# Kernel tuning notes

Hardware: AMD Instinct MI355X
Metric: run time of the kernel (lower is better)

Reference implementation:

```python
import jax, jax.numpy as jnp
import numpy as np

NUM_ENT = 14541; NUM_REL = 237; NUM_EDGES = 544230
D = 200; B = 2048
IPERM = 1; IK_H = 20; IK_W = 10; NFILT = 96; KER = 9
FLAT = IK_H * 2 * IK_W * NFILT * IPERM
LEAKY = 0.2; EPS = 1e-5


def _chequer_perm(rng):
    # faithful reimplementation of RagatInteractE.get_chequer_perm
    ent_perm = np.stack([rng.permutation(D) for _ in range(IPERM)])
    rel_perm = np.stack([rng.permutation(D) for _ in range(IPERM)])
    comb = []
    for k in range(IPERM):
        temp = []; ei = 0; ri = 0
        for i in range(IK_H):
            for j in range(IK_W):
                ent_first = (k % 2 == 0) == (i % 2 == 0)
                if ent_first:
                    temp.append(ent_perm[k, ei]); ei += 1
                    temp.append(rel_perm[k, ri] + D); ri += 1
                else:
                    temp.append(rel_perm[k, ri] + D); ri += 1
                    temp.append(ent_perm[k, ei]); ei += 1
        comb.append(temp)
    return jnp.asarray(np.asarray(comb, dtype=np.int32))


def _bn1d(x, g, b):  # [N, C], training-mode batch stats (torch default)
    m = x.mean(0); v = x.var(0)
    return (x - m) / jnp.sqrt(v + EPS) * g + b


def _bn2d(x, g, b):  # [N, C, H, W]
    m = x.mean((0, 2, 3), keepdims=True); v = x.var((0, 2, 3), keepdims=True)
    return (x - m) / jnp.sqrt(v + EPS) * g[None, :, None, None] + b[None, :, None, None]


def _seg_softmax_agg(score, msg, seg, n):
    # segment softmax over edges grouped by destination node, then weighted scatter-add
    mx = jax.ops.segment_max(score, seg, num_segments=n)
    ex = jnp.exp(score - mx[seg])
    den = jax.ops.segment_sum(ex, seg, num_segments=n)
    alpha = ex / (den[seg] + 1e-16)
    return jax.ops.segment_sum(msg * alpha[:, None], seg, num_segments=n)


def setup_inputs() -> dict:
    key = jax.random.key(0)
    ks = jax.random.split(key, 20)
    f = lambda k, shp, s=0.1: jax.random.normal(k, shp, jnp.float32) * s
    rng = np.random.RandomState(0)
    return {
        'init_embed': f(ks[0], (NUM_ENT, D)),
        'init_rel': f(ks[1], (2 * NUM_REL, D)),
        'loop_rel': f(ks[2], (1, D)),
        'w_in': f(ks[3], (D, D)),
        'w_out': f(ks[4], (D, D)),
        'w_loop': f(ks[5], (D, D)),
        'w_rel': f(ks[6], (D, D)),
        'att_in': f(ks[7], (D,)),
        'att_out': f(ks[8], (D,)),
        'bn_conv_g': jnp.ones((D,), jnp.float32),
        'bn_conv_b': jnp.zeros((D,), jnp.float32),
        'conv_filt': f(ks[9], (NFILT, 1, KER, KER)),
        'bn0_g': jnp.ones((IPERM,), jnp.float32),
        'bn0_b': jnp.zeros((IPERM,), jnp.float32),
        'bn1_g': jnp.ones((NFILT * IPERM,), jnp.float32),
        'bn1_b': jnp.zeros((NFILT * IPERM,), jnp.float32),
        'fc_w': f(ks[10], (FLAT, D), 0.02),
        'fc_b': jnp.zeros((D,), jnp.float32),
        'bn2_g': jnp.ones((D,), jnp.float32),
        'bn2_b': jnp.zeros((D,), jnp.float32),
        'bias': jnp.zeros((NUM_ENT,), jnp.float32),
        'edge_index': jax.random.randint(ks[11], (2, NUM_EDGES), 0, NUM_ENT, jnp.int32),
        'edge_type': jnp.concatenate([
            jax.random.randint(ks[12], (NUM_EDGES // 2,), 0, NUM_REL, jnp.int32),
            jax.random.randint(ks[13], (NUM_EDGES // 2,), NUM_REL, 2 * NUM_REL, jnp.int32)]),
        'sub': jax.random.randint(ks[14], (B,), 0, NUM_ENT, jnp.int32),
        'rel': jax.random.randint(ks[15], (B,), 0, 2 * NUM_REL, jnp.int32),
        'chequer_perm': _chequer_perm(rng),
    }


def reference(init_embed, init_rel, loop_rel, w_in, w_out, w_loop, w_rel,
              att_in, att_out, bn_conv_g, bn_conv_b, conv_filt,
              bn0_g, bn0_b, bn1_g, bn1_b, fc_w, fc_b, bn2_g, bn2_b, bias,
              edge_index, edge_type, sub, rel, chequer_perm):
    # --- RagatConv (1 layer): relation-aware composition + edge attention + scatter-agg ---
    rel_full = jnp.concatenate([init_rel, loop_rel], 0)
    src, dst = edge_index[0], edge_index[1]
    comp = init_embed[dst] * rel_full[edge_type]          # [E, D] mult composition
    half = NUM_EDGES // 2
    msg_in = comp[:half] @ w_in                           # [E/2, D]
    msg_out = comp[half:] @ w_out
    s_in = jax.nn.leaky_relu((msg_in * att_in).sum(-1), LEAKY)
    s_out = jax.nn.leaky_relu((msg_out * att_out).sum(-1), LEAKY)
    agg_in = _seg_softmax_agg(s_in, msg_in, src[:half], NUM_ENT)
    agg_out = _seg_softmax_agg(s_out, msg_out, src[half:], NUM_ENT)
    loop_msg = (init_embed * loop_rel[0]) @ w_loop
    ent = (agg_in + agg_out + loop_msg) / 3.0
    ent = jnp.tanh(_bn1d(ent, bn_conv_g, bn_conv_b))      # [num_ent, D]
    rel_out = init_rel @ w_rel                            # [2*num_rel, D]

    # --- InteractE chequer-perm circular-conv scoring ---
    comb = jnp.concatenate([ent[sub], rel_out[rel]], 1)   # [B, 2D]
    cheq = comb[:, chequer_perm]                          # [B, IPERM, 2D]
    x = cheq.reshape(B, IPERM, 2 * IK_W, IK_H)
    x = _bn2d(x, bn0_g, bn0_b)
    p = KER // 2
    x = jnp.concatenate([x[..., -p:, :], x, x[..., :p, :]], axis=2)  # circular pad H
    x = jnp.concatenate([x[..., -p:], x, x[..., :p]], axis=3)        # circular pad W
    kern = jnp.tile(conv_filt, (IPERM, 1, 1, 1))          # [NFILT*IPERM, 1, K, K]
    x = jax.lax.conv_general_dilated(x, kern, (1, 1), 'VALID',
                                     dimension_numbers=('NCHW', 'OIHW', 'NCHW'),
                                     feature_group_count=IPERM)       # [B, 96, 20, 20]
    x = jax.nn.relu(_bn2d(x, bn1_g, bn1_b))
    x = x.reshape(B, FLAT)
    x = x @ fc_w + fc_b
    x = jax.nn.relu(_bn1d(x, bn2_g, bn2_b))               # [B, D]
    scores = x @ ent.T + bias                              # one_to_n scoring
    return jax.nn.sigmoid(scores)
```

## Files before the change

kernel.cpp:

```cpp
#include <hip/hip_runtime.h>
#include <hip/hip_bf16.h>

constexpr int DV     = 200;
constexpr int N_ENT  = 14541;
constexpr int N_EDGE = 544230;
constexpr int HALF_E = N_EDGE / 2;
constexpr int NSEG   = 2 * N_ENT;
constexpr int BB     = 2048;
constexpr int NF     = 96;
constexpr int FLATN  = 38400;
constexpr float LEAK = 0.2f;
constexpr float BEPS = 1e-5f;

typedef unsigned int u32;
typedef unsigned short u16;
typedef __attribute__((ext_vector_type(8))) short bf16x8;
typedef __attribute__((ext_vector_type(4))) float f32x4;
typedef __attribute__((ext_vector_type(4))) unsigned short u16x4;

constexpr size_t OFF_S    = 0;
constexpr size_t OFF_EID  = 544230;
constexpr size_t OFF_CNT  = 1088460;
constexpr size_t OFF_OFFS = 1117542;
constexpr size_t OFF_AGG  = 1146624;
constexpr size_t OFF_FC   = 6963218;
constexpr size_t ZERO_BEG = OFF_CNT;
constexpr size_t ZERO_END = OFF_FC + 409600;
constexpr size_t OFF_V    = 7372818;
constexpr size_t OFF_WTH  = 0;
constexpr size_t OFF_ENTH = 3840000;
constexpr size_t OFF_ENTL = 5352264;
constexpr size_t OFF_WTL  = 7373220;
constexpr size_t OFF_EPRE = 10281418;
constexpr size_t OFF_ENT  = 13189618;
constexpr size_t OFF_RELO = 16097818;
constexpr size_t OFF_CM   = 16192618;
constexpr size_t OFF_CV   = 16192818;
constexpr size_t OFF_CHEQ = 16193018;
constexpr size_t OFF_WT3H = 16193018;
constexpr size_t OFF_WT3L = 16261118;
constexpr size_t OFF_YH   = 16193020;
constexpr size_t OFF_YL   = 16406012;
constexpr size_t OFF_P0   = 17012218;
constexpr size_t OFF_ST0  = 17016314;
constexpr size_t OFF_CHP  = 17016316;
constexpr size_t OFF_B1SC = 17409532;
constexpr size_t OFF_B1BI = 17409628;
constexpr size_t OFF_XC   = 17819324;
constexpr size_t WS_WORDS = OFF_XC + 39321600;

__device__ inline float bf2f(u16 u) { return __uint_as_float(((u32)u) << 16); }
__device__ inline u16 f2bf(float f) {
    __hip_bfloat16 h = __float2bfloat16(f);
    return *reinterpret_cast<u16*>(&h);
}
__device__ inline void gl_lds16(const void* g, void* l) {
    __builtin_amdgcn_global_load_lds(
        (const __attribute__((address_space(1))) void*)g,
        (__attribute__((address_space(3))) void*)l, 16, 0, 0);
}

__global__ void k_vatt(const float* __restrict__ w_in, const float* __restrict__ w_out,
                       const float* __restrict__ att_in, const float* __restrict__ att_out,
                       float* __restrict__ v) {
    int t = blockIdx.x * 256 + threadIdx.x;
    if (t < DV) {
        float s = 0.f;
        for (int j = 0; j < DV; ++j) s += w_in[t * DV + j] * att_in[j];
        v[t] = s;
    } else if (t < 2 * DV) {
        int k = t - DV;
        float s = 0.f;
        for (int j = 0; j < DV; ++j) s += w_out[k * DV + j] * att_out[j];
        v[t] = s;
    }
}

__global__ void k_edge_score(const float* __restrict__ embed, const float* __restrict__ rel,
                             const int* __restrict__ eidx, const int* __restrict__ etype,
                             const float* __restrict__ v, float* __restrict__ s_all) {
    int gw = (blockIdx.x * 256 + threadIdx.x) >> 6;
    int lane = threadIdx.x & 63;
    if (gw >= N_EDGE) return;
    int e = gw;
    int dst = eidx[N_EDGE + e], et = etype[e];
    int dir = (e >= HALF_E);
    const float* vv = v + dir * DV;
    const float* er = embed + (size_t)dst * DV;
    const float* rr = rel + (size_t)et * DV;
    float acc = 0.f;
    for (int d = lane; d < DV; d += 64) acc += er[d] * rr[d] * vv[d];
    for (int off = 32; off > 0; off >>= 1) acc += __shfl_down(acc, off);
    if (lane == 0) {
        float s = acc > 0.f ? acc : LEAK * acc;
        s_all[e] = s;
    }
}

__global__ void k_hist(const int* __restrict__ eidx, u32* __restrict__ cnt) {
    int e = blockIdx.x * 256 + threadIdx.x;
    if (e >= N_EDGE) return;
    int seg = (e >= HALF_E ? N_ENT : 0) + eidx[e];
    atomicAdd(&cnt[seg], 1u);
}

__global__ void k_scan(u32* __restrict__ cnt, u32* __restrict__ offs) {
    __shared__ u32 s[256];
    __shared__ u32 base;
    if (threadIdx.x == 0) base = 0;
    __syncthreads();
    for (int c0 = 0; c0 < NSEG; c0 += 256) {
        int i = c0 + threadIdx.x;
        u32 vv = (i < NSEG) ? cnt[i] : 0;
        s[threadIdx.x] = vv;
        __syncthreads();
        for (int o = 1; o < 256; o <<= 1) {
            u32 t = (threadIdx.x >= (u32)o) ? s[threadIdx.x - o] : 0u;
            __syncthreads();
            s[threadIdx.x] += t;
            __syncthreads();
        }
        u32 exc = base + s[threadIdx.x] - vv;
        if (i < NSEG) { offs[i] = exc; cnt[i] = exc; }
        __syncthreads();
        if (threadIdx.x == 255) base += s[255];
        __syncthreads();
    }
}

__global__ void k_scatter(const int* __restrict__ eidx, u32* __restrict__ pos,
                          u32* __restrict__ eid) {
    int e = blockIdx.x * 256 + threadIdx.x;
    if (e >= N_EDGE) return;
    int seg = (e >= HALF_E ? N_ENT : 0) + eidx[e];
    u32 slot = atomicAdd(&pos[seg], 1u);
    eid[slot] = (u32)e;
}

__global__ void k_seg_agg(const float* __restrict__ embed, const float* __restrict__ rel,
                          const int* __restrict__ eidx, const int* __restrict__ etype,
                          const float* __restrict__ s_all, const u32* __restrict__ offs,
                          const u32* __restrict__ eid, float* __restrict__ aggC) {
    int gw = (blockIdx.x * 256 + threadIdx.x) >> 6;
    int lane = threadIdx.x & 63;
    if (gw >= NSEG) return;
    u32 beg = offs[gw];
    u32 end = (gw == NSEG - 1) ? (u32)N_EDGE : offs[gw + 1];
    int deg = (int)(end - beg);
    if (deg == 0) return;
    float m = -1e30f;
    for (int i = lane; i < deg; i += 64) m = fmaxf(m, s_all[eid[beg + i]]);
    for (int o = 32; o > 0; o >>= 1) m = fmaxf(m, __shfl_xor(m, o));
    float dsum = 0.f;
    for (int i = lane; i < deg; i += 64) dsum += expf(s_all[eid[beg + i]] - m);
    for (int o = 32; o > 0; o >>= 1) dsum += __shfl_xor(dsum, o);
    float inv = 1.f / (dsum + 1e-16f);
    float a0 = 0.f, a1 = 0.f, a2 = 0.f, a3 = 0.f;
    bool t3 = (lane < 8);
    for (int j = 0; j < deg; ++j) {
        int e = (int)eid[beg + j];
        float alpha = expf(s_all[e] - m) * inv;
        int dst = eidx[N_EDGE + e], et = etype[e];
        const float* er = embed + (size_t)dst * DV;
        const float* rr = rel + (size_t)et * DV;
        float p0 = er[lane] * rr[lane];
        float p1 = er[lane + 64] * rr[lane + 64];
        float p2 = er[lane + 128] * rr[lane + 128];
        float p3 = t3 ? er[lane + 192] * rr[lane + 192] : 0.f;
        a0 = fmaf(p0, alpha, a0);
        a1 = fmaf(p1, alpha, a1);
        a2 = fmaf(p2, alpha, a2);
        a3 = fmaf(p3, alpha, a3);
    }
    float* ag = aggC + (size_t)gw * DV;
    ag[lane] = a0;
    ag[lane + 64] = a1;
    ag[lane + 128] = a2;
    if (t3) ag[lane + 192] = a3;
}

__global__ void gemm_nn(const float* __restrict__ A, const float* __restrict__ B,
                        float* __restrict__ C, int M, int N, int K, int beta) {
    __shared__ float As[16][65];
    __shared__ float Bs[16][64];
    int bm = blockIdx.x * 64, bn = blockIdx.y * 64;
    int tx = threadIdx.x & 15, ty = threadIdx.x >> 4;
    float acc[4][4] = {};
    for (int k0 = 0; k0 < K; k0 += 16) {
        for (int i = threadIdx.x; i < 1024; i += 256) {
            int m = i >> 4, k = i & 15;
            int gm = bm + m, gk = k0 + k;
            As[k][m] = (gm < M && gk < K) ? A[(size_t)gm * K + gk] : 0.f;
        }
        for (int i = threadIdx.x; i < 1024; i += 256) {
            int k = i >> 6, n = i & 63;
            int gk = k0 + k, gn = bn + n;
            Bs[k][n] = (gk < K && gn < N) ? B[(size_t)gk * N + gn] : 0.f;
        }
        __syncthreads();
#pragma unroll
        for (int k = 0; k < 16; ++k) {
            float a[4], bv[4];
#pragma unroll
            for (int i = 0; i < 4; i++) a[i] = As[k][ty * 4 + i];
#pragma unroll
            for (int j = 0; j < 4; j++) bv[j] = Bs[k][tx * 4 + j];
#pragma unroll
            for (int i = 0; i < 4; i++)
#pragma unroll
                for (int j = 0; j < 4; j++) acc[i][j] += a[i] * bv[j];
        }
        __syncthreads();
    }
#pragma unroll
    for (int i = 0; i < 4; i++) {
        int r = bm + ty * 4 + i;
        if (r >= M) continue;
#pragma unroll
        for (int j = 0; j < 4; j++) {
            int c = bn + tx * 4 + j;
            if (c >= N) continue;
            size_t idx = (size_t)r * N + c;
            C[idx] = beta ? C[idx] + acc[i][j] : acc[i][j];
        }
    }
}

__global__ void k_wt3(const float* __restrict__ w_in, const float* __restrict__ w_out,
                      const float* __restrict__ w_loop,
                      u16* __restrict__ wTh, u16* __restrict__ wTl) {
    int i = blockIdx.x * 256 + threadIdx.x;
    if (i >= 3 * 200 * 224) return;
    int s = i / 44800, rem = i - s * 44800;
    int n = rem / 224, k = rem - n * 224;
    const float* w = (s == 0) ? w_in : (s == 1 ? w_out : w_loop);
    float v = (k < 200) ? w[k * 200 + n] : 0.f;
    u16 h = f2bf(v);
    wTh[i] = h;
    wTl[i] = f2bf(v - bf2f(h));
}

__global__ __launch_bounds__(256) void k_epre_mfma(const float* __restrict__ aggC,
        const float* __restrict__ embed, const float* __restrict__ lr,
        const u16* __restrict__ wTh, const u16* __restrict__ wTl,
        float* __restrict__ epre) {
    __shared__ __align__(16) char elds[26624];
    int tid = threadIdx.x;
    int w = tid >> 6, lane = tid & 63;
    int lrow = lane & 15, lkg = lane >> 4;
    int mw = blockIdx.x * 128 + w * 32;
    f32x4 acc[2][13] = {};
    for (int seg = 0; seg < 3; ++seg) {
        const float* Asrc = (seg == 0) ? aggC : (seg == 1 ? aggC + (size_t)N_ENT * DV : embed);
        const u16* bhg = wTh + seg * 44800;
        const u16* blg = wTl + seg * 44800;
        for (int kt = 0; kt < 7; ++kt) {
            int kb = kt * 32;
            __syncthreads();
            int kk = kb + lkg * 8;
            bool kval = (kt < 6) || (lkg < 1);
            bf16x8 ah[2], al[2];
#pragma unroll
            for (int mf = 0; mf < 2; ++mf) {
                int r = mw + mf * 16 + lrow; if (r > N_ENT - 1) r = N_ENT - 1;
                bf16x8 vh = {}, vl = {};
                if (kval) {
                    const float* ap = Asrc + (size_t)r * DV + kk;
#pragma unroll
                    for (int j = 0; j < 8; ++j) {
                        float v = ap[j];
                        if (seg == 2) v *= lr[kk + j];
                        u16 h = f2bf(v);
                        vh[j] = (short)h;
                        vl[j] = (short)f2bf(v - bf2f(h));
                    }
                }
                ah[mf] = vh; al[mf] = vl;
            }
#pragma unroll
            for (int q = 0; q < 4; ++q) {
                int bidx = q * 256 + w * 64;
                if (bidx < 832) {
                    int idx = bidx + lane;
                    int n = idx >> 2;
                    int slot = (idx & 3) ^ (n & 3);
                    size_t gsrc = (size_t)n * 224 + kb + slot * 8;
                    gl_lds16(bhg + gsrc, elds + bidx * 16);
                    gl_lds16(blg + gsrc, elds + 13312 + bidx * 16);
                }
            }
            __syncthreads();
#pragma unroll
            for (int nt = 0; nt < 13; ++nt) {
                int n = nt * 16 + lrow;
                int off = n * 64 + ((lkg ^ (n & 3)) << 4);
                bf16x8 bh = *reinterpret_cast<const bf16x8*>(elds + off);
                bf16x8 bl = *reinterpret_cast<const bf16x8*>(elds + 13312 + off);
#pragma unroll
                for (int mf = 0; mf < 2; ++mf) {
                    acc[mf][nt] = __builtin_amdgcn_mfma_f32_16x16x32_bf16(ah[mf], bh, acc[mf][nt], 0, 0, 0);
                    acc[mf][nt] = __builtin_amdgcn_mfma_f32_16x16x32_bf16(ah[mf], bl, acc[mf][nt], 0, 0, 0);
                    acc[mf][nt] = __builtin_amdgcn_mfma_f32_16x16x32_bf16(al[mf], bh, acc[mf][nt], 0, 0, 0);
                }
            }
        }
    }
#pragma unroll
    for (int mf = 0; mf < 2; ++mf)
#pragma unroll
        for (int nt = 0; nt < 13; ++nt) {
            int col = nt * 16 + lrow;
            if (col < DV) {
#pragma unroll
                for (int i = 0; i < 4; ++i) {
                    int r = mw + mf * 16 + lkg * 4 + i;
                    if (r < N_ENT) epre[(size_t)r * DV + col] = acc[mf][nt][i];
                }
            }
        }
}

__global__ void k_colstats(const float* __restrict__ X, int R,
                           float* __restrict__ cm, float* __restrict__ cv) {
    int col = blockIdx.x;
    __shared__ float rs[256], rss[256];
    float s = 0.f, ss = 0.f;
    for (int r = threadIdx.x; r < R; r += 256) {
        float x = X[(size_t)r * DV + col];
        s += x; ss += x * x;
    }
    rs[threadIdx.x] = s; rss[threadIdx.x] = ss;
    __syncthreads();
    for (int o = 128; o > 0; o >>= 1) {
        if (threadIdx.x < o) { rs[threadIdx.x] += rs[threadIdx.x + o]; rss[threadIdx.x] += rss[threadIdx.x + o]; }
        __syncthreads();
    }
    if (threadIdx.x == 0) {
        float m = rs[0] / R;
        cm[col] = m;
        cv[col] = rss[0] / R - m * m;
    }
}

__global__ void k_bn_ent(const float* __restrict__ epre, const float* __restrict__ cm,
                         const float* __restrict__ cv, const float* __restrict__ g,
                         const float* __restrict__ b, float* __restrict__ ent,
                         u16* __restrict__ eh, u16* __restrict__ el) {
    size_t i = (size_t)blockIdx.x * 256 + threadIdx.x;
    if (i >= (size_t)N_ENT * 208) return;
    int row = (int)(i / 208), col = (int)(i % 208);
    if (col < DV) {
        float val = (epre[(size_t)row * DV + col] - cm[col]) * rsqrtf(cv[col] + 9.f * BEPS) * g[col] + b[col];
        val = tanhf(val);
        ent[(size_t)row * DV + col] = val;
        u16 h = f2bf(val);
        eh[i] = h;
        el[i] = f2bf(val - bf2f(h));
    } else { eh[i] = 0; el[i] = 0; }
}

__global__ void k_bn2y(const float* __restrict__ fc, const float* __restrict__ cm,
                       const float* __restrict__ cv, const float* __restrict__ g,
                       const float* __restrict__ b, u16* __restrict__ yh,
                       u16* __restrict__ yl) {
    size_t i = (size_t)blockIdx.x * 256 + threadIdx.x;
    if (i >= (size_t)BB * 208) return;
    int row = (int)(i / 208), col = (int)(i % 208);
    if (col < DV) {
        float val = (fc[(size_t)row * DV + col] - cm[col]) * rsqrtf(cv[col] + BEPS) * g[col] + b[col];
        val = fmaxf(val, 0.f);
        u16 h = f2bf(val);
        yh[i] = h;
        yl[i] = f2bf(val - bf2f(h));
    } else { yh[i] = 0; yl[i] = 0; }
}

__global__ __launch_bounds__(256) void k_wt(const float* __restrict__ W,
                                            u16* __restrict__ Wth, u16* __restrict__ Wtl) {
    __shared__ float lds[64][65];
    int k0 = blockIdx.x * 64, n0 = blockIdx.y * 64;
    for (int idx = threadIdx.x; idx < 4096; idx += 256) {
        int kl = idx >> 6, nl = idx & 63;
        int gk = k0 + kl, gn = n0 + nl;
        lds[kl][nl] = (gn < DV) ? W[(size_t)gk * DV + gn] : 0.f;
    }
    __syncthreads();
    int nl = threadIdx.x >> 2, kq = threadIdx.x & 3;
    int gn = n0 + nl;
    if (gn >= DV) return;
    size_t base = (size_t)gn * FLATN + k0 + kq * 16;
    bf16x8 vh0, vh1, vl0, vl1;
#pragma unroll
    for (int j = 0; j < 8; ++j) {
        float w0 = lds[kq * 16 + j][nl];
        u16 h0 = f2bf(w0);
        vh0[j] = (short)h0; vl0[j] = (short)f2bf(w0 - bf2f(h0));
        float w1 = lds[kq * 16 + 8 + j][nl];
        u16 h1 = f2bf(w1);
        vh1[j] = (short)h1; vl1[j] = (short)f2bf(w1 - bf2f(h1));
    }
    *reinterpret_cast<bf16x8*>(Wth + base)     = vh0;
    *reinterpret_cast<bf16x8*>(Wth + base + 8) = vh1;
    *reinterpret_cast<bf16x8*>(Wtl + base)     = vl0;
    *reinterpret_cast<bf16x8*>(Wtl + base + 8) = vl1;
}

__global__ void k_cheq(const float* __restrict__ ent, const float* __restrict__ rel_out,
                       const int* __restrict__ sub, const int* __restrict__ rel,
                       const int* __restrict__ perm, float* __restrict__ cheq,
                       float* __restrict__ p0) {
    int b = blockIdx.x;
    int sb = sub[b], rb = rel[b];
    __shared__ float rs[256], rss[256];
    float s = 0.f, ss = 0.f;
    for (int i = threadIdx.x; i < 400; i += 256) {
        int p = perm[i];
        float v = (p < DV) ? ent[(size_t)sb * DV + p] : rel_out[(size_t)rb * DV + (p - DV)];
        cheq[(size_t)b * 400 + i] = v;
        s += v; ss += v * v;
    }
    rs[threadIdx.x] = s; rss[threadIdx.x] = ss;
    __syncthreads();
    for (int o = 128; o > 0; o >>= 1) {
        if (threadIdx.x < o) { rs[threadIdx.x] += rs[threadIdx.x + o]; rss[threadIdx.x] += rss[threadIdx.x + o]; }
        __syncthreads();
    }
    if (threadIdx.x == 0) { p0[b] = rs[0]; p0[BB + b] = rss[0]; }
}

__global__ void k_red_bn0(const float* __restrict__ p0, float* __restrict__ st) {
    __shared__ float rs[256], rss[256];
    float s = 0.f, ss = 0.f;
    for (int i = threadIdx.x; i < BB; i += 256) { s += p0[i]; ss += p0[BB + i]; }
    rs[threadIdx.x] = s; rss[threadIdx.x] = ss;
    __syncthreads();
    for (int o = 128; o > 0; o >>= 1) {
        if (threadIdx.x < o) { rs[threadIdx.x] += rs[threadIdx.x + o]; rss[threadIdx.x] += rss[threadIdx.x + o]; }
        __syncthreads();
    }
    if (threadIdx.x == 0) { st[0] = rs[0]; st[1] = rss[0]; }
}

__global__ __launch_bounds__(384, 4) void k_conv(const float* __restrict__ cheq,
                                              const float* __restrict__ st,
                                              const float* __restrict__ g0, const float* __restrict__ b0,
                                              const float* __restrict__ filt,
                                              __hip_bfloat16* __restrict__ xconv,
                                              float* __restrict__ chp) {
    int t = threadIdx.x;
    int img = t / 192;
    int tl = t - img * 192;
    int b = blockIdx.x * 2 + img;
    __shared__ float pad[2][784];
    __shared__ float flds[7968];
    __shared__ float red[384];
    for (int i = t; i < 7776; i += 384) {
        int f = i / 81, q = i - f * 81;
        flds[f * 83 + q] = filt[i];
    }
    const float N0 = (float)BB * 400.f;
    float m = st[0] / N0;
    float va = st[1] / N0 - m * m;
    float sg = rsqrtf(va + BEPS) * g0[0];
    float sb = b0[0] - m * sg;
    for (int i = t; i < 1568; i += 384) {
        int im = i / 784, j = i - im * 784;
        int h = j / 28, w2 = j % 28;
        int r = (h + 16) % 20, c = (w2 + 16) % 20;
        pad[im][j] = cheq[(size_t)(blockIdx.x * 2 + im) * 400 + r * 20 + c] * sg + sb;
    }
    __syncthreads();
    int f = tl % 96, hp = tl / 96;
    const float* fbase = flds + f * 83;
    const float* mypad = pad[img];
    float cs = 0.f, css = 0.f;
    u16* xo = (u16*)xconv + (size_t)b * FLATN + f * 400 + hp * 200;
    for (int rt = 0; rt < 10; ++rt) {
        int y = hp * 10 + rt;
        float acc[20];
#pragma unroll
        for (int x = 0; x < 20; ++x) acc[x] = 0.f;
        for (int dy = 0; dy < 9; ++dy) {
            float pr[28];
            const float4* prow = reinterpret_cast<const float4*>(&mypad[(y + dy) * 28]);
#pragma unroll
            for (int qv = 0; qv < 7; ++qv) {
                float4 v4 = prow[qv];
                pr[qv * 4 + 0] = v4.x; pr[qv * 4 + 1] = v4.y;
                pr[qv * 4 + 2] = v4.z; pr[qv * 4 + 3] = v4.w;
            }
            float fw[9];
#pragma unroll
            for (int dx = 0; dx < 9; ++dx) fw[dx] = fbase[dy * 9 + dx];
#pragma unroll
            for (int dx = 0; dx < 9; ++dx)
#pragma unroll
                for (int x = 0; x < 20; ++x)
                    acc[x] = fmaf(pr[x + dx], fw[dx], acc[x]);
        }
#pragma unroll
        for (int x = 0; x < 20; ++x) { cs += acc[x]; css += acc[x] * acc[x]; }
#pragma unroll
        for (int jj = 0; jj < 5; ++jj) {
            u16x4 o;
#pragma unroll
            for (int q2 = 0; q2 < 4; ++q2) o[q2] = f2bf(acc[jj * 4 + q2]);
            *reinterpret_cast<u16x4*>(xo + rt * 20 + jj * 4) = o;
        }
    }
    red[t] = cs; __syncthreads();
    if (tl < 96) chp[(size_t)b * 192 + tl] = red[img * 192 + tl] + red[img * 192 + tl + 96];
    __syncthreads();
    red[t] = css; __syncthreads();
    if (tl < 96) chp[(size_t)b * 192 + 96 + tl] = red[img * 192 + tl] + red[img * 192 + tl + 96];
}

__global__ void k_bn1_final(const float* __restrict__ chp, const float* __restrict__ g1,
                            const float* __restrict__ b1, float* __restrict__ sc,
                            float* __restrict__ bi) {
    int c = blockIdx.x;
    __shared__ float rs[256], rss[256];
    float s = 0.f, ss = 0.f;
    for (int b = threadIdx.x; b < BB; b += 256) {
        s += chp[(size_t)b * 192 + c];
        ss += chp[(size_t)b * 192 + 96 + c];
    }
    rs[threadIdx.x] = s; rss[threadIdx.x] = ss;
    __syncthreads();
    for (int o = 128; o > 0; o >>= 1) {
        if (threadIdx.x < o) { rs[threadIdx.x] += rs[threadIdx.x + o]; rss[threadIdx.x] += rss[threadIdx.x + o]; }
        __syncthreads();
    }
    if (threadIdx.x == 0) {
        float N = (float)BB * 400.f;
        float m = rs[0] / N;
        float v = rss[0] / N - m * m;
        float s_ = rsqrtf(v + BEPS) * g1[c];
        sc[c] = s_;
        bi[c] = b1[c] - m * s_;
    }
}

__global__ __launch_bounds__(256) void k_fc_mfma(const u16* __restrict__ X,
        const u16* __restrict__ Wth, const u16* __restrict__ Wtl,
        const float* __restrict__ sc, const float* __restrict__ bi,
        float* __restrict__ outp) {
    __shared__ __align__(16) char blds[53248];
    int tid = threadIdx.x;
    int w = tid >> 6, lane = tid & 63;
    int lrow = lane & 15, lkg = lane >> 4;
    int mw = blockIdx.x * 128 + w * 32;
    int kbase = blockIdx.y * 1280;
    f32x4 acc[2][13] = {};
    for (int it = 0; it < 20; ++it) {
        int k0 = kbase + it * 64;
        __syncthreads();
        bf16x8 araw[2][2];
#pragma unroll
        for (int mf = 0; mf < 2; ++mf)
#pragma unroll
            for (int kt = 0; kt < 2; ++kt) {
                int r = mw + mf * 16 + lrow;
                int kk = k0 + kt * 32 + lkg * 8;
                araw[mf][kt] = *reinterpret_cast<const bf16x8*>(X + (size_t)r * FLATN + kk);
            }
#pragma unroll
        for (int q = 0; q < 7; ++q) {
            int bidx = q * 256 + w * 64;
            if (bidx < 1600) {
                int idx = bidx + lane;
                int n = idx >> 3;
                int slot = (idx & 7) ^ (n & 7);
                size_t gsrc = (size_t)n * FLATN + k0 + slot * 8;
                gl_lds16(Wth + gsrc, blds + bidx * 16);
                gl_lds16(Wtl + gsrc, blds + 26624 + bidx * 16);
            }
        }
        bf16x8 ah[2][2], al[2][2];
#pragma unroll
        for (int mf = 0; mf < 2; ++mf)
#pragma unroll
            for (int kt = 0; kt < 2; ++kt) {
                int kk = k0 + kt * 32 + lkg * 8;
                int c = kk / 400;
                float s_ = sc[c], b_ = bi[c];
                bf16x8 fh2, fl2;
#pragma unroll
                for (int j = 0; j < 8; ++j) {
                    float v = bf2f((u16)araw[mf][kt][j]);
                    v = fmaxf(fmaf(v, s_, b_), 0.f);
                    u16 h = f2bf(v);
                    fh2[j] = (short)h;
                    fl2[j] = (short)f2bf(v - bf2f(h));
                }
                ah[mf][kt] = fh2;
                al[mf][kt] = fl2;
            }
        __syncthreads();
#pragma unroll
        for (int nt = 0; nt < 13; ++nt) {
            int n = nt * 16 + lrow;
            int row = n * 128, nx = n & 7;
            int off0 = row + ((lkg ^ nx) << 4);
            int off1 = row + (((4 + lkg) ^ nx) << 4);
            bf16x8 bh0 = *reinterpret_cast<const bf16x8*>(blds + off0);
            bf16x8 bh1 = *reinterpret_cast<const bf16x8*>(blds + off1);
            bf16x8 bl0 = *reinterpret_cast<const bf16x8*>(blds + 26624 + off0);
            bf16x8 bl1 = *reinterpret_cast<const bf16x8*>(blds + 26624 + off1);
#pragma unroll
            for (int mf = 0; mf < 2; ++mf) {
                acc[mf][nt] = __builtin_amdgcn_mfma_f32_16x16x32_bf16(ah[mf][0], bh0, acc[mf][nt], 0, 0, 0);
                acc[mf][nt] = __builtin_amdgcn_mfma_f32_16x16x32_bf16(ah[mf][1], bh1, acc[mf][nt], 0, 0, 0);
                acc[mf][nt] = __builtin_amdgcn_mfma_f32_16x16x32_bf16(ah[mf][0], bl0, acc[mf][nt], 0, 0, 0);
                acc[mf][nt] = __builtin_amdgcn_mfma_f32_16x16x32_bf16(ah[mf][1], bl1, acc[mf][nt], 0, 0, 0);
                acc[mf][nt] = __builtin_amdgcn_mfma_f32_16x16x32_bf16(al[mf][0], bh0, acc[mf][nt], 0, 0, 0);
                acc[mf][nt] = __builtin_amdgcn_mfma_f32_16x16x32_bf16(al[mf][1], bh1, acc[mf][nt], 0, 0, 0);
            }
        }
    }
#pragma unroll
    for (int mf = 0; mf < 2; ++mf)
#pragma unroll
        for (int nt = 0; nt < 13; ++nt) {
            int col = nt * 16 + lrow;
            if (col < DV) {
#pragma unroll
                for (int i = 0; i < 4; ++i) {
                    int r = mw + mf * 16 + lkg * 4 + i;
                    unsafeAtomicAdd(&outp[(size_t)r * DV + col], acc[mf][nt][i]);
                }
            }
        }
}

__global__ __launch_bounds__(256) void k_sc_mfma(const u16* __restrict__ Yh, const u16* __restrict__ Yl,
        const u16* __restrict__ Eh, const u16* __restrict__ El,
        const float* __restrict__ bias, float* __restrict__ outp) {
    __shared__ __align__(16) char elds[32768];
    int tid = threadIdx.x;
    int w = tid >> 6, lane = tid & 63;
    int lrow = lane & 15, lkg = lane >> 4;
    int mw = blockIdx.x * 128 + w * 32;
    int bn = blockIdx.y * 256;
    f32x4 acc[2][16] = {};
    bf16x8 zv = {};
    for (int kt = 0; kt < 7; ++kt) {
        int kbase = kt * 32;
        __syncthreads();
        int kk = kbase + lkg * 8;
        bool kval = (kt < 6) || (lkg < 2);
        bf16x8 ah[2], al[2];
#pragma unroll
        for (int mf = 0; mf < 2; ++mf) {
            int r = mw + mf * 16 + lrow;
            size_t off = (size_t)r * 208 + kk;
            ah[mf] = kval ? *reinterpret_cast<const bf16x8*>(Yh + off) : zv;
            al[mf] = kval ? *reinterpret_cast<const bf16x8*>(Yl + off) : zv;
        }
#pragma unroll
        for (int q = 0; q < 4; ++q) {
            int bidx = q * 256 + w * 64;
            int idx = bidx + lane;
            int n = idx >> 2;
            int slot = (idx & 3) ^ (n & 3);
            int gn = bn + n; if (gn > N_ENT - 1) gn = N_ENT - 1;
            size_t gsrc = (size_t)gn * 208 + kbase + slot * 8;
            gl_lds16(Eh + gsrc, elds + bidx * 16);
            gl_lds16(El + gsrc, elds + 16384 + bidx * 16);
        }
        __syncthreads();
#pragma unroll
        for (int nt = 0; nt < 16; ++nt) {
            int n = nt * 16 + lrow;
            int off = n * 64 + ((lkg ^ (n & 3)) << 4);
            bf16x8 bh = *reinterpret_cast<const bf16x8*>(elds + off);
            bf16x8 bl = *reinterpret_cast<const bf16x8*>(elds + 16384 + off);
            acc[0][nt] = __builtin_amdgcn_mfma_f32_16x16x32_bf16(ah[0], bh, acc[0][nt], 0, 0, 0);
            acc[0][nt] = __builtin_amdgcn_mfma_f32_16x16x32_bf16(ah[0], bl, acc[0][nt], 0, 0, 0);
            acc[0][nt] = __builtin_amdgcn_mfma_f32_16x16x32_bf16(al[0], bh, acc[0][nt], 0, 0, 0);
            acc[1][nt] = __builtin_amdgcn_mfma_f32_16x16x32_bf16(ah[1], bh, acc[1][nt], 0, 0, 0);
            acc[1][nt] = __builtin_amdgcn_mfma_f32_16x16x32_bf16(ah[1], bl, acc[1][nt], 0, 0, 0);
            acc[1][nt] = __builtin_amdgcn_mfma_f32_16x16x32_bf16(al[1], bh, acc[1][nt], 0, 0, 0);
        }
    }
#pragma unroll
    for (int mf = 0; mf < 2; ++mf)
#pragma unroll
        for (int nt = 0; nt < 16; ++nt) {
            int col = bn + nt * 16 + lrow;
            if (col < N_ENT) {
                float bv = bias[col];
#pragma unroll
                for (int i = 0; i < 4; ++i) {
                    int r = mw + mf * 16 + lkg * 4 + i;
                    float s = acc[mf][nt][i] + bv;
                    outp[(size_t)r * N_ENT + col] = 1.f / (1.f + expf(-s));
                }
            }
        }
}

extern "C" void kernel_launch(void* const* d_in, const int* in_sizes, int n_in,
                              void* d_out, int out_size, void* d_ws, size_t ws_size,
                              hipStream_t stream) {
    const float* init_embed = (const float*)d_in[0];
    const float* init_rel   = (const float*)d_in[1];
    const float* loop_rel   = (const float*)d_in[2];
    const float* w_in   = (const float*)d_in[3];
    const float* w_out  = (const float*)d_in[4];
    const float* w_loop = (const float*)d_in[5];
    const float* w_rel  = (const float*)d_in[6];
    const float* att_in  = (const float*)d_in[7];
    const float* att_out = (const float*)d_in[8];
    const float* bnc_g = (const float*)d_in[9];
    const float* bnc_b = (const float*)d_in[10];
    const float* filt  = (const float*)d_in[11];
    const float* g0 = (const float*)d_in[12];
    const float* b0 = (const float*)d_in[13];
    const float* g1 = (const float*)d_in[14];
    const float* b1 = (const float*)d_in[15];
    const float* fc_w = (const float*)d_in[16];
    const float* g2 = (const float*)d_in[18];
    const float* b2 = (const float*)d_in[19];
    const float* bias = (const float*)d_in[20];
    const int* eidx  = (const int*)d_in[21];
    const int* etype = (const int*)d_in[22];
    const int* sub   = (const int*)d_in[23];
    const int* rel   = (const int*)d_in[24];
    const int* perm  = (const int*)d_in[25];

    float* ws = (float*)d_ws;
    float* outp = (float*)d_out;
    if (ws_size < WS_WORDS * sizeof(float)) return;

    float* s_all  = ws + OFF_S;
    u32*   eid    = (u32*)(ws + OFF_EID);
    u32*   cnt    = (u32*)(ws + OFF_CNT);
    u32*   offs   = (u32*)(ws + OFF_OFFS);
    float* aggC   = ws + OFF_AGG;
    float* fc_out = ws + OFF_FC;
    float* v      = ws + OFF_V;
    float* epre   = ws + OFF_EPRE;
    float* ent    = ws + OFF_ENT;
    float* relo   = ws + OFF_RELO;
    float* cm     = ws + OFF_CM;
    float* cv     = ws + OFF_CV;
    float* cheq   = ws + OFF_CHEQ;
    float* p0     = ws + OFF_P0;
    float* st0    = ws + OFF_ST0;
    float* chp    = ws + OFF_CHP;
    float* b1sc   = ws + OFF_B1SC;
    float* b1bi   = ws + OFF_B1BI;
    u16*   Wth    = (u16*)(ws + OFF_WTH);
    u16*   Wtl    = (u16*)(ws + OFF_WTL);
    u16*   wT3h   = (u16*)(ws + OFF_WT3H);
    u16*   wT3l   = (u16*)(ws + OFF_WT3L);
    u16*   entH   = (u16*)(ws + OFF_ENTH);
    u16*   entL   = (u16*)(ws + OFF_ENTL);
    u16*   Yh     = (u16*)(ws + OFF_YH);
    u16*   Yl     = (u16*)(ws + OFF_YL);
    __hip_bfloat16* xconv = (__hip_bfloat16*)(ws + OFF_XC);

    hipMemsetAsync(ws + ZERO_BEG, 0, (ZERO_END - ZERO_BEG) * sizeof(float), stream);

    k_vatt<<<2, 256, 0, stream>>>(w_in, w_out, att_in, att_out, v);
    k_wt3<<<(3 * 200 * 224 + 255) / 256, 256, 0, stream>>>(w_in, w_out, w_loop, wT3h, wT3l);

    int edge_wave_blocks = (N_EDGE + 3) / 4;
    k_edge_score<<<edge_wave_blocks, 256, 0, stream>>>(init_embed, init_rel, eidx, etype, v, s_all);

    int eb = (N_EDGE + 255) / 256;
    k_hist<<<eb, 256, 0, stream>>>(eidx, cnt);
    k_scan<<<1, 256, 0, stream>>>(cnt, offs);
    k_scatter<<<eb, 256, 0, stream>>>(eidx, cnt, eid);
    k_seg_agg<<<(NSEG + 3) / 4, 256, 0, stream>>>(init_embed, init_rel, eidx, etype,
                                                  s_all, offs, eid, aggC);

    k_epre_mfma<<<(N_ENT + 127) / 128, 256, 0, stream>>>(aggC, init_embed, loop_rel,
                                                         wT3h, wT3l, epre);

    dim3 gR((474 + 63) / 64, (DV + 63) / 64);
    gemm_nn<<<gR, 256, 0, stream>>>(init_rel, w_rel, relo, 474, DV, DV, 0);

    k_colstats<<<DV, 256, 0, stream>>>(epre, N_ENT, cm, cv);
    k_bn_ent<<<((size_t)N_ENT * 208 + 255) / 256, 256, 0, stream>>>(
        epre, cm, cv, bnc_g, bnc_b, ent, entH, entL);

    dim3 gW(FLATN / 64, 4);
    k_wt<<<gW, 256, 0, stream>>>(fc_w, Wth, Wtl);

    k_cheq<<<BB, 256, 0, stream>>>(ent, relo, sub, rel, perm, cheq, p0);
    k_red_bn0<<<1, 256, 0, stream>>>(p0, st0);
    k_conv<<<BB / 2, 384, 0, stream>>>(cheq, st0, g0, b0, filt, xconv, chp);
    k_bn1_final<<<NF, 256, 0, stream>>>(chp, g1, b1, b1sc, b1bi);

    dim3 gFC(16, 30);
    k_fc_mfma<<<gFC, 256, 0, stream>>>((const u16*)xconv, Wth, Wtl, b1sc, b1bi, fc_out);

    k_colstats<<<DV, 256, 0, stream>>>(fc_out, BB, cm, cv);
    k_bn2y<<<((size_t)BB * 208 + 255) / 256, 256, 0, stream>>>(fc_out, cm, cv, g2, b2, Yh, Yl);

    dim3 gS(16, 57);
    k_sc_mfma<<<gS, 256, 0, stream>>>(Yh, Yl, entH, entL, bias, outp);
}
```

Measured before the change: 1.152 ms.

## Double-buffer LDS weight tiles in FC and scoring MFMA GEMMs

Both the FC GEMM and the entity-scoring GEMM now prefetch the next K-slice of the B operand into a second LDS buffer while the current slice is consumed by MFMAs, with one barrier per iteration instead of two. The FC kernel halves its K step to 32 so the two buffers fit in the existing 53 KB LDS array, and clamps the row index to avoid reading past row 199. The scoring kernel doubles its LDS to 64 KB, which may reduce occupancy, and the FC kernel now runs twice as many iterations, adding per-iteration overhead.

```diff
diff --git a/kernel.cpp b/kernel.cpp
--- a/kernel.cpp
+++ b/kernel.cpp
@@ -552,71 +552,73 @@
     int mw = blockIdx.x * 128 + w * 32;
     int kbase = blockIdx.y * 1280;
     f32x4 acc[2][13] = {};
-    for (int it = 0; it < 20; ++it) {
-        int k0 = kbase + it * 64;
-        __syncthreads();
-        bf16x8 araw[2][2];
-#pragma unroll
-        for (int mf = 0; mf < 2; ++mf)
-#pragma unroll
-            for (int kt = 0; kt < 2; ++kt) {
-                int r = mw + mf * 16 + lrow;
-                int kk = k0 + kt * 32 + lkg * 8;
-                araw[mf][kt] = *reinterpret_cast<const bf16x8*>(X + (size_t)r * FLATN + kk);
-            }
-#pragma unroll
-        for (int q = 0; q < 7; ++q) {
-            int bidx = q * 256 + w * 64;
-            if (bidx < 1600) {
-                int idx = bidx + lane;
-                int n = idx >> 3;
-                int slot = (idx & 7) ^ (n & 7);
-                size_t gsrc = (size_t)n * FLATN + k0 + slot * 8;
-                gl_lds16(Wth + gsrc, blds + bidx * 16);
-                gl_lds16(Wtl + gsrc, blds + 26624 + bidx * 16);
-            }
-        }
-        bf16x8 ah[2][2], al[2][2];
-#pragma unroll
-        for (int mf = 0; mf < 2; ++mf)
-#pragma unroll
-            for (int kt = 0; kt < 2; ++kt) {
-                int kk = k0 + kt * 32 + lkg * 8;
-                int c = kk / 400;
-                float s_ = sc[c], b_ = bi[c];
-                bf16x8 fh2, fl2;
-#pragma unroll
-                for (int j = 0; j < 8; ++j) {
-                    float v = bf2f((u16)araw[mf][kt][j]);
-                    v = fmaxf(fmaf(v, s_, b_), 0.f);
-                    u16 h = f2bf(v);
-                    fh2[j] = (short)h;
-                    fl2[j] = (short)f2bf(v - bf2f(h));
+#pragma unroll
+    for (int q = 0; q < 4; ++q) {
+        int bidx = q * 256 + w * 64;
+        if (bidx < 832) {
+            int idx = bidx + lane;
+            int n = idx >> 2; if (n > 199) n = 199;
+            int slot = (idx & 3) ^ (n & 3);
+            size_t gsrc = (size_t)n * FLATN + kbase + slot * 8;
+            gl_lds16(Wth + gsrc, blds + bidx * 16);
+            gl_lds16(Wtl + gsrc, blds + 13312 + bidx * 16);
+        }
+    }
+    __syncthreads();
+    int cur = 0;
+    for (int it = 0; it < 40; ++it) {
+        int k0 = kbase + it * 32;
+        if (it + 1 < 40) {
+            int ob = (cur ^ 1) * 26624;
+            int kn = k0 + 32;
+#pragma unroll
+            for (int q = 0; q < 4; ++q) {
+                int bidx = q * 256 + w * 64;
+                if (bidx < 832) {
+                    int idx = bidx + lane;
+                    int n = idx >> 2; if (n > 199) n = 199;
+                    int slot = (idx & 3) ^ (n & 3);
+                    size_t gsrc = (size_t)n * FLATN + kn + slot * 8;
+                    gl_lds16(Wth + gsrc, blds + ob + bidx * 16);
+                    gl_lds16(Wtl + gsrc, blds + ob + 13312 + bidx * 16);
                 }
-                ah[mf][kt] = fh2;
-                al[mf][kt] = fl2;
-            }
-        __syncthreads();
+            }
+        }
+        int kk = k0 + lkg * 8;
+        int c = kk / 400;
+        float s_ = sc[c], b_ = bi[c];
+        bf16x8 ah[2], al[2];
+#pragma unroll
+        for (int mf = 0; mf < 2; ++mf) {
+            int r = mw + mf * 16 + lrow;
+            bf16x8 raw = *reinterpret_cast<const bf16x8*>(X + (size_t)r * FLATN + kk);
+            bf16x8 fh2, fl2;
+#pragma unroll
+            for (int j = 0; j < 8; ++j) {
+                float v = bf2f((u16)raw[j]);
+                v = fmaxf(fmaf(v, s_, b_), 0.f);
+                u16 h = f2bf(v);
+                fh2[j] = (short)h;
+                fl2[j] = (short)f2bf(v - bf2f(h));
+            }
+            ah[mf] = fh2; al[mf] = fl2;
+        }
+        int cb = cur * 26624;
 #pragma unroll
         for (int nt = 0; nt < 13; ++nt) {
             int n = nt * 16 + lrow;
-            int row = n * 128, nx = n & 7;
-            int off0 = row + ((lkg ^ nx) << 4);
-            int off1 = row + (((4 + lkg) ^ nx) << 4);
-            bf16x8 bh0 = *reinterpret_cast<const bf16x8*>(blds + off0);
-            bf16x8 bh1 = *reinterpret_cast<const bf16x8*>(blds + off1);
-            bf16x8 bl0 = *reinterpret_cast<const bf16x8*>(blds + 26624 + off0);
-            bf16x8 bl1 = *reinterpret_cast<const bf16x8*>(blds + 26624 + off1);
+            int off = cb + n * 64 + ((lkg ^ (n & 3)) << 4);
+            bf16x8 bh = *reinterpret_cast<const bf16x8*>(blds + off);
+            bf16x8 bl = *reinterpret_cast<const bf16x8*>(blds + off + 13312);
 #pragma unroll
             for (int mf = 0; mf < 2; ++mf) {
-                acc[mf][nt] = __builtin_amdgcn_mfma_f32_16x16x32_bf16(ah[mf][0], bh0, acc[mf][nt], 0, 0, 0);
-                acc[mf][nt] = __builtin_amdgcn_mfma_f32_16x16x32_bf16(ah[mf][1], bh1, acc[mf][nt], 0, 0, 0);
-                acc[mf][nt] = __builtin_amdgcn_mfma_f32_16x16x32_bf16(ah[mf][0], bl0, acc[mf][nt], 0, 0, 0);
-                acc[mf][nt] = __builtin_amdgcn_mfma_f32_16x16x32_bf16(ah[mf][1], bl1, acc[mf][nt], 0, 0, 0);
-                acc[mf][nt] = __builtin_amdgcn_mfma_f32_16x16x32_bf16(al[mf][0], bh0, acc[mf][nt], 0, 0, 0);
-                acc[mf][nt] = __builtin_amdgcn_mfma_f32_16x16x32_bf16(al[mf][1], bh1, acc[mf][nt], 0, 0, 0);
-            }
-        }
+                acc[mf][nt] = __builtin_amdgcn_mfma_f32_16x16x32_bf16(ah[mf], bh, acc[mf][nt], 0, 0, 0);
+                acc[mf][nt] = __builtin_amdgcn_mfma_f32_16x16x32_bf16(ah[mf], bl, acc[mf][nt], 0, 0, 0);
+                acc[mf][nt] = __builtin_amdgcn_mfma_f32_16x16x32_bf16(al[mf], bh, acc[mf][nt], 0, 0, 0);
+            }
+        }
+        __syncthreads();
+        cur ^= 1;
     }
 #pragma unroll
     for (int mf = 0; mf < 2; ++mf)
@@ -636,7 +638,7 @@
 __global__ __launch_bounds__(256) void k_sc_mfma(const u16* __restrict__ Yh, const u16* __restrict__ Yl,
         const u16* __restrict__ Eh, const u16* __restrict__ El,
         const float* __restrict__ bias, float* __restrict__ outp) {
-    __shared__ __align__(16) char elds[32768];
+    __shared__ __align__(16) char elds[65536];
     int tid = threadIdx.x;
     int w = tid >> 6, lane = tid & 63;
     int lrow = lane & 15, lkg = lane >> 4;
@@ -644,9 +646,36 @@
     int bn = blockIdx.y * 256;
     f32x4 acc[2][16] = {};
     bf16x8 zv = {};
+#pragma unroll
+    for (int q = 0; q < 4; ++q) {
+        int bidx = q * 256 + w * 64;
+        int idx = bidx + lane;
+        int n = idx >> 2;
+        int slot = (idx & 3) ^ (n & 3);
+        int gn = bn + n; if (gn > N_ENT - 1) gn = N_ENT - 1;
+        size_t gsrc = (size_t)gn * 208 + slot * 8;
+        gl_lds16(Eh + gsrc, elds + bidx * 16);
+        gl_lds16(El + gsrc, elds + 16384 + bidx * 16);
+    }
+    __syncthreads();
+    int cur = 0;
     for (int kt = 0; kt < 7; ++kt) {
         int kbase = kt * 32;
-        __syncthreads();
+        if (kt + 1 < 7) {
+            int ob = (cur ^ 1) * 32768;
+            int kn = kbase + 32;
+#pragma unroll
+            for (int q = 0; q < 4; ++q) {
+                int bidx = q * 256 + w * 64;
+                int idx = bidx + lane;
+                int n = idx >> 2;
+                int slot = (idx & 3) ^ (n & 3);
+                int gn = bn + n; if (gn > N_ENT - 1) gn = N_ENT - 1;
+                size_t gsrc = (size_t)gn * 208 + kn + slot * 8;
+                gl_lds16(Eh + gsrc, elds + ob + bidx * 16);
+                gl_lds16(El + gsrc, elds + ob + 16384 + bidx * 16);
+            }
+        }
         int kk = kbase + lkg * 8;
         bool kval = (kt < 6) || (lkg < 2);
         bf16x8 ah[2], al[2];
@@ -657,24 +686,13 @@
             ah[mf] = kval ? *reinterpret_cast<const bf16x8*>(Yh + off) : zv;
             al[mf] = kval ? *reinterpret_cast<const bf16x8*>(Yl + off) : zv;
         }
-#pragma unroll
-        for (int q = 0; q < 4; ++q) {
-            int bidx = q * 256 + w * 64;
-            int idx = bidx + lane;
-            int n = idx >> 2;
-            int slot = (idx & 3) ^ (n & 3);
-            int gn = bn + n; if (gn > N_ENT - 1) gn = N_ENT - 1;
-            size_t gsrc = (size_t)gn * 208 + kbase + slot * 8;
-            gl_lds16(Eh + gsrc, elds + bidx * 16);
-            gl_lds16(El + gsrc, elds + 16384 + bidx * 16);
-        }
-        __syncthreads();
+        int cb = cur * 32768;
 #pragma unroll
         for (int nt = 0; nt < 16; ++nt) {
             int n = nt * 16 + lrow;
-            int off = n * 64 + ((lkg ^ (n & 3)) << 4);
+            int off = cb + n * 64 + ((lkg ^ (n & 3)) << 4);
             bf16x8 bh = *reinterpret_cast<const bf16x8*>(elds + off);
-            bf16x8 bl = *reinterpret_cast<const bf16x8*>(elds + 16384 + off);
+            bf16x8 bl = *reinterpret_cast<const bf16x8*>(elds + off + 16384);
             acc[0][nt] = __builtin_amdgcn_mfma_f32_16x16x32_bf16(ah[0], bh, acc[0][nt], 0, 0, 0);
             acc[0][nt] = __builtin_amdgcn_mfma_f32_16x16x32_bf16(ah[0], bl, acc[0][nt], 0, 0, 0);
             acc[0][nt] = __builtin_amdgcn_mfma_f32_16x16x32_bf16(al[0], bh, acc[0][nt], 0, 0, 0);
@@ -682,6 +700,8 @@
             acc[1][nt] = __builtin_amdgcn_mfma_f32_16x16x32_bf16(ah[1], bl, acc[1][nt], 0, 0, 0);
             acc[1][nt] = __builtin_amdgcn_mfma_f32_16x16x32_bf16(al[1], bh, acc[1][nt], 0, 0, 0);
         }
+        __syncthreads();
+        cur ^= 1;
     }
 #pragma unroll
     for (int mf = 0; mf < 2; ++mf)
```

Measured after the change: 1.159 ms. Within noise of the previous version (+0.6%).
